# Kernel optimization log

Hardware: AMD Instinct MI355X
Metric: run time of the kernel (lower is better)

Reference implementation:

```python
import jax, jax.numpy as jnp
import numpy as np

B, S, D = 2, 2048, 1024
H, HD = 16, 64


def setup_inputs() -> dict:
    key = jax.random.key(0)
    ks = jax.random.split(key, 10)
    scale = 1.0 / np.sqrt(D)
    inputs_q = jax.random.normal(ks[0], (B, S, D), dtype=jnp.float32)
    inputs_kv = jax.random.normal(ks[1], (B, S, D), dtype=jnp.float32)
    # causal mask, broadcast over batch: True = attend
    mask = jnp.broadcast_to(jnp.tril(jnp.ones((S, S), dtype=bool)), (B, S, S))
    Wq = jax.random.normal(ks[2], (D, H * HD), dtype=jnp.float32) * scale
    bq = jnp.zeros((H * HD,), dtype=jnp.float32)
    Wk = jax.random.normal(ks[3], (D, H * HD), dtype=jnp.float32) * scale
    bk = jnp.zeros((H * HD,), dtype=jnp.float32)
    Wv = jax.random.normal(ks[4], (D, H * HD), dtype=jnp.float32) * scale
    bv = jnp.zeros((H * HD,), dtype=jnp.float32)
    Wo = jax.random.normal(ks[5], (H * HD, D), dtype=jnp.float32) * scale
    bo = jnp.zeros((D,), dtype=jnp.float32)
    return {"inputs_q": inputs_q, "inputs_kv": inputs_kv, "mask": mask,
            "Wq": Wq, "bq": bq, "Wk": Wk, "bk": bk, "Wv": Wv, "bv": bv,
            "Wo": Wo, "bo": bo}


def reference(inputs_q, inputs_kv, mask, Wq, bq, Wk, bk, Wv, bv, Wo, bo):
    b, s_q, _ = inputs_q.shape
    s_k = inputs_kv.shape[1]
    # projections -> [B, S, H, HD]
    q = (inputs_q @ Wq + bq).reshape(b, s_q, H, HD)
    k = (inputs_kv @ Wk + bk).reshape(b, s_k, H, HD)
    v = (inputs_kv @ Wv + bv).reshape(b, s_k, H, HD)
    q = q / jnp.sqrt(jnp.asarray(HD, dtype=q.dtype))
    # scores: [B, H, Sq, Sk]
    attn = jnp.einsum('bqhd,bkhd->bhqk', q, k)
    m = mask[:, None, :, :]  # [B,1,Sq,Sk] broadcast over heads
    attn = jnp.where(m, attn, jnp.asarray(-1e30, dtype=attn.dtype))
    attn = jax.nn.softmax(attn, axis=-1)
    # dropout_rate = 0.0, deterministic -> identity
    out = jnp.einsum('bhqk,bkhd->bqhd', attn, v).reshape(b, s_q, H * HD)
    return out @ Wo + bo
```

## Files before the change

### kernel.cpp

```cpp
#include <hip/hip_runtime.h>

typedef __attribute__((ext_vector_type(4))) float f32x4;
typedef __attribute__((ext_vector_type(8))) short bf16x8;
typedef unsigned short u16;
typedef unsigned int u32;

#define AS1 __attribute__((address_space(1)))
#define AS3 __attribute__((address_space(3)))

#define WAITVM(N) do{ asm volatile("s_waitcnt vmcnt(" #N ")" ::: "memory"); \
                      __builtin_amdgcn_sched_barrier(0); }while(0)
#define RAWBAR    do{ __builtin_amdgcn_s_barrier();                          \
                      __builtin_amdgcn_sched_barrier(0); }while(0)

__device__ __forceinline__ float fast_exp2(float x){
  return __builtin_amdgcn_exp2f(x);
}

__device__ __forceinline__ u16 f2bf(float x){
  u32 u = __float_as_uint(x);
  u += 0x7fffu + ((u >> 16) & 1u);
  return (u16)(u >> 16);
}
__device__ __forceinline__ u16 f2bf_fast(float x){
  return (u16)((__float_as_uint(x) + 0x8000u) >> 16);
}

__global__ __launch_bounds__(256) void prep(const float* __restrict__ W0,
                                            const float* __restrict__ W1,
                                            const float* __restrict__ W2,
                                            const float* __restrict__ W3,
                                            u16* __restrict__ Wt,
                                            const float* __restrict__ inq,
                                            const float* __restrict__ inkv,
                                            u16* __restrict__ Xq,
                                            u16* __restrict__ Xkv)
{
  const int z = blockIdx.z;
  if (z < 4){
    __shared__ float tile[32][33];
    const float* src = z == 0 ? W0 : z == 1 ? W1 : z == 2 ? W2 : W3;
    u16* d = Wt + (size_t)z * 1024 * 1024;
    int tx = threadIdx.x & 31, ty = threadIdx.x >> 5;
    int k0 = blockIdx.x * 32, n0 = blockIdx.y * 32;
    for (int r = 0; r < 4; ++r)
      tile[ty + r * 8][tx] = src[(size_t)(k0 + ty + r * 8) * 1024 + n0 + tx];
    __syncthreads();
    for (int r = 0; r < 4; ++r)
      d[(size_t)(n0 + ty + r * 8) * 1024 + k0 + tx] = f2bf(tile[tx][ty + r * 8]);
  } else {
    const float* src = z == 4 ? inq : inkv;
    u16* dst = z == 4 ? Xq : Xkv;
    int bid = blockIdx.y * 32 + blockIdx.x;
    size_t base4 = ((size_t)bid * 256 + threadIdx.x) * 4;
#pragma unroll
    for (int i = 0; i < 4; ++i){
      float4 v = reinterpret_cast<const float4*>(src)[base4 + i];
      ushort4 o;
      o.x = f2bf(v.x); o.y = f2bf(v.y); o.z = f2bf(v.z); o.w = f2bf(v.w);
      reinterpret_cast<ushort4*>(dst)[base4 + i] = o;
    }
  }
}

__global__ __launch_bounds__(512, 2) void gemm_qkv(const u16* __restrict__ Xq,
                                                   const u16* __restrict__ Xkv,
                                                   const u16* __restrict__ Wt,
                                                   const float* __restrict__ bq,
                                                   const float* __restrict__ bk,
                                                   const float* __restrict__ bv,
                                                   u16* __restrict__ Qb,
                                                   u16* __restrict__ Kb,
                                                   u16* __restrict__ Vt,
                                                   int M, int K)
{
  __shared__ u16 lA[3][256 * 32];
  __shared__ u16 lB[3][256 * 32];
  const int tid = threadIdx.x;
  const int l = tid & 63, w = tid >> 6;
  const int wr = w >> 2, wc = w & 3;
  const int bm0 = blockIdx.x * 256, bn0 = blockIdx.y * 256;
  const int seg = bn0 >> 10;
  const int nloc0 = bn0 & 1023;
  const u16* A = seg ? Xkv : Xq;
  const float* bias = seg == 0 ? bq : seg == 1 ? bk : bv;
  const float scale = seg == 0 ? 0.125f * 1.44269504089f : 1.0f;
  const int lr = l & 15, lg = (l >> 4) * 8;

#define STAGE_G(BI, KK) do{                                                   \
  _Pragma("unroll") for (int c_ = 0; c_ < 2; ++c_){                           \
    int e_ = (c_ * 512 + tid) * 8;                                            \
    int row_ = e_ >> 5, col_ = e_ & 31;                                       \
    __builtin_amdgcn_global_load_lds(                                         \
        (const AS1 u32*)(A + (size_t)(bm0 + row_) * K + (KK) * 32 + col_),    \
        (AS3 u32*)(&lA[BI][e_]), 16, 0, 0);                                   \
    __builtin_amdgcn_global_load_lds(                                         \
        (const AS1 u32*)(Wt + (size_t)(bn0 + row_) * K + (KK) * 32 + col_),   \
        (AS3 u32*)(&lB[BI][e_]), 16, 0, 0);                                   \
  }                                                                           \
}while(0)

  f32x4 acc[8][4];
#pragma unroll
  for (int m = 0; m < 8; ++m)
#pragma unroll
    for (int n = 0; n < 4; ++n) acc[m][n] = (f32x4){0.f, 0.f, 0.f, 0.f};

  STAGE_G(0, 0);
  STAGE_G(1, 1);

#pragma unroll
  for (int k = 0; k < 32; ++k){
    const int cur = k % 3;
    if (k < 30){ STAGE_G((k + 2) % 3, k + 2); WAITVM(8); }
    else if (k == 30){ WAITVM(4); }
    else { WAITVM(0); }
    RAWBAR;

    bf16x8 aF[8], bF[4];
#pragma unroll
    for (int m = 0; m < 8; ++m)
      aF[m] = *reinterpret_cast<const bf16x8*>(&lA[cur][(wr * 128 + m * 16 + lr) * 32 + lg]);
#pragma unroll
    for (int n = 0; n < 4; ++n)
      bF[n] = *reinterpret_cast<const bf16x8*>(&lB[cur][(wc * 64 + n * 16 + lr) * 32 + lg]);
    __builtin_amdgcn_s_setprio(1);
#pragma unroll
    for (int m = 0; m < 8; ++m)
#pragma unroll
      for (int n = 0; n < 4; ++n)
        acc[m][n] = __builtin_amdgcn_mfma_f32_16x16x32_bf16(aF[m], bF[n], acc[m][n], 0, 0, 0);
    __builtin_amdgcn_s_setprio(0);
    RAWBAR;
  }
#undef STAGE_G

  const int r0 = (l >> 4) * 4;
  if (seg < 2){
    u16* C = seg == 0 ? Qb : Kb;
#pragma unroll
    for (int m = 0; m < 8; ++m)
#pragma unroll
      for (int n = 0; n < 4; ++n){
        int col = nloc0 + wc * 64 + n * 16 + lr;
        float bv_ = bias[col];
#pragma unroll
        for (int r = 0; r < 4; ++r){
          int row = bm0 + wr * 128 + m * 16 + r0 + r;
          C[(size_t)row * 1024 + col] = f2bf((acc[m][n][r] + bv_) * scale);
        }
      }
  } else {
#pragma unroll
    for (int m = 0; m < 8; ++m)
#pragma unroll
      for (int n = 0; n < 4; ++n){
        int col = nloc0 + wc * 64 + n * 16 + lr;
        float bv_ = bias[col];
        int h = col >> 6, hdl = col & 63;
#pragma unroll
        for (int r = 0; r < 4; ++r){
          int row = bm0 + wr * 128 + m * 16 + r0 + r;
          int b = row >> 11, kv = row & 2047;
          size_t off = ((size_t)(b * 16 + h)) * 131072 + (size_t)hdl * 2048 + kv;
          Vt[off] = f2bf(acc[m][n][r] + bv_);
        }
      }
  }
}

__global__ __launch_bounds__(256) void gemm_out(const u16* __restrict__ A,
                                                const u16* __restrict__ Bt,
                                                const float* __restrict__ bias,
                                                float* __restrict__ Cf,
                                                int M, int N, int K)
{
  __shared__ u16 lA[3][64 * 32];
  __shared__ u16 lB[3][128 * 32];
  const int tid = threadIdx.x;
  const int l = tid & 63, w = tid >> 6;
  const int wr = w >> 1, wc = w & 1;
  const int bm0 = blockIdx.x * 64, bn0 = blockIdx.y * 128;
  const int lr = l & 15, lg = (l >> 4) * 8;

#define STAGE_O(BI, KK) do{                                                   \
  {                                                                           \
    int e_ = tid * 8;                                                         \
    int row_ = e_ >> 5, col_ = e_ & 31;                                       \
    __builtin_amdgcn_global_load_lds(                                         \
        (const AS1 u32*)(A + (size_t)(bm0 + row_) * K + (KK) * 32 + col_),    \
        (AS3 u32*)(&lA[BI][e_]), 16, 0, 0);                                   \
  }                                                                           \
  _Pragma("unroll") for (int c_ = 0; c_ < 2; ++c_){                           \
    int e_ = (c_ * 256 + tid) * 8;                                            \
    int row_ = e_ >> 5, col_ = e_ & 31;                                       \
    __builtin_amdgcn_global_load_lds(                                         \
        (const AS1 u32*)(Bt + (size_t)(bn0 + row_) * K + (KK) * 32 + col_),   \
        (AS3 u32*)(&lB[BI][e_]), 16, 0, 0);                                   \
  }                                                                           \
}while(0)

  f32x4 acc[2][4];
#pragma unroll
  for (int m = 0; m < 2; ++m)
#pragma unroll
    for (int n = 0; n < 4; ++n) acc[m][n] = (f32x4){0.f, 0.f, 0.f, 0.f};

  STAGE_O(0, 0);
  STAGE_O(1, 1);

#pragma unroll
  for (int k = 0; k < 32; ++k){
    const int cur = k % 3;
    if (k < 30){ STAGE_O((k + 2) % 3, k + 2); WAITVM(6); }
    else if (k == 30){ WAITVM(3); }
    else { WAITVM(0); }
    RAWBAR;

    bf16x8 aF[2], bF[4];
#pragma unroll
    for (int m = 0; m < 2; ++m)
      aF[m] = *reinterpret_cast<const bf16x8*>(&lA[cur][(wr * 32 + m * 16 + lr) * 32 + lg]);
#pragma unroll
    for (int n = 0; n < 4; ++n)
      bF[n] = *reinterpret_cast<const bf16x8*>(&lB[cur][(wc * 64 + n * 16 + lr) * 32 + lg]);
    __builtin_amdgcn_s_setprio(1);
#pragma unroll
    for (int m = 0; m < 2; ++m)
#pragma unroll
      for (int n = 0; n < 4; ++n)
        acc[m][n] = __builtin_amdgcn_mfma_f32_16x16x32_bf16(aF[m], bF[n], acc[m][n], 0, 0, 0);
    __builtin_amdgcn_s_setprio(0);
    RAWBAR;
  }
#undef STAGE_O

  const int r0 = (l >> 4) * 4;
#pragma unroll
  for (int m = 0; m < 2; ++m)
#pragma unroll
    for (int n = 0; n < 4; ++n){
      int col = bn0 + wc * 64 + n * 16 + lr;
      float bv_ = bias[col];
#pragma unroll
      for (int r = 0; r < 4; ++r){
        int row = bm0 + wr * 32 + m * 16 + r0 + r;
        Cf[(size_t)row * N + col] = acc[m][n][r] + bv_;
      }
    }
}

__global__ __launch_bounds__(512, 2) void attn_fwd(const u16* __restrict__ Qb,
                                                   const u16* __restrict__ Kb,
                                                   const u16* __restrict__ Vt,
                                                   u16* __restrict__ AO, int S)
{
  __shared__ u16 lK[2][64 * 64];
  __shared__ u16 lV[2][64 * 64];
  __shared__ u16 lP[8][16 * 72];
  const int tid = threadIdx.x, l = tid & 63, w = tid >> 6;
  const int j = blockIdx.x;
  const int xcd = j & 7;
  const int bh = xcd * 4 + ((j >> 3) & 3);
  const int p = j >> 5;
  const int bb = bh >> 4;
  const size_t baseQK = ((size_t)bb * S) * 1024 + (bh & 15) * 64;
  const u16* gK = Kb + baseQK;
  const u16* gV = Vt + (size_t)bh * 131072;
  const int lr = l & 15, g4 = l >> 4, lg = g4 * 8;

  u16* lPw = (u16*)lP[w];
  bf16x8 ones;
#pragma unroll
  for (int i = 0; i < 8; ++i) ones[i] = (short)0x3F80;

#define STAGE_KV(T, BI) do{                                                   \
  int row_ = tid >> 3, ch_ = tid & 7, sc_ = (ch_ ^ (row_ & 7)) * 8;           \
  __builtin_amdgcn_global_load_lds(                                           \
      (const AS1 u32*)(gK + (size_t)(64 * (T) + row_) * 1024 + sc_),          \
      (AS3 u32*)(&lK[BI][tid * 8]), 16, 0, 0);                                \
  __builtin_amdgcn_global_load_lds(                                           \
      (const AS1 u32*)(gV + (size_t)row_ * 2048 + 64 * (T) + sc_),            \
      (AS3 u32*)(&lV[BI][tid * 8]), 16, 0, 0);                                \
}while(0)

#pragma unroll
  for (int pass = 0; pass < 2; ++pass){
    const int qt = pass ? (15 - p) : p;
    const int ntb = 2 * qt + 2;
    const int q0 = qt * 128 + w * 16;

    bf16x8 qf[2];
#pragma unroll
    for (int kc = 0; kc < 2; ++kc)
      qf[kc] = *reinterpret_cast<const bf16x8*>(
          Qb + baseQK + (size_t)(q0 + lr) * 1024 + kc * 32 + lg);

    f32x4 acc_o[4], acc_l;
    acc_l = (f32x4){0.f, 0.f, 0.f, 0.f};
#pragma unroll
    for (int n = 0; n < 4; ++n) acc_o[n] = (f32x4){0.f, 0.f, 0.f, 0.f};

    int buf = 0;
    STAGE_KV(0, 0);
    for (int t = 0; t < ntb; ++t){
      if (t + 1 < ntb){ STAGE_KV(t + 1, buf ^ 1); WAITVM(2); }
      else            { WAITVM(0); }
      RAWBAR;

      if (64 * t <= q0 + 15){
        const u16* lKb = lK[buf];
        const u16* lVb = lV[buf];
        f32x4 sA[4];
#pragma unroll
        for (int np = 0; np < 4; ++np) sA[np] = (f32x4){0.f, 0.f, 0.f, 0.f};
        __builtin_amdgcn_s_setprio(1);
#pragma unroll
        for (int kc = 0; kc < 2; ++kc)
#pragma unroll
          for (int np = 0; np < 4; ++np){
            int row = np * 16 + lr, ch = kc * 4 + g4;
            bf16x8 kf = *reinterpret_cast<const bf16x8*>(
                reinterpret_cast<const char*>(lKb) + row * 128 + ((ch ^ (row & 7)) << 4));
            sA[np] = __builtin_amdgcn_mfma_f32_16x16x32_bf16(qf[kc], kf, sA[np], 0, 0, 0);
          }
        __builtin_amdgcn_s_setprio(0);

        const bool needmask = (64 * t + 63 > q0);
        if (needmask){
#pragma unroll
          for (int np = 0; np < 4; ++np){
            int kvg = 64 * t + np * 16 + lr;
#pragma unroll
            for (int r = 0; r < 4; ++r){
              int qg = q0 + g4 * 4 + r;
              float e = fast_exp2(sA[np][r]);
              lPw[(g4 * 4 + r) * 72 + np * 16 + lr] = f2bf_fast((kvg <= qg) ? e : 0.f);
            }
          }
        } else {
#pragma unroll
          for (int np = 0; np < 4; ++np)
#pragma unroll
            for (int r = 0; r < 4; ++r)
              lPw[(g4 * 4 + r) * 72 + np * 16 + lr] = f2bf_fast(fast_exp2(sA[np][r]));
        }

        bf16x8 pf[2];
#pragma unroll
        for (int kc = 0; kc < 2; ++kc)
          pf[kc] = *reinterpret_cast<const bf16x8*>(
              reinterpret_cast<const char*>(lPw) + lr * 144 + (kc * 4 + g4) * 16);
        __builtin_amdgcn_s_setprio(1);
#pragma unroll
        for (int kc = 0; kc < 2; ++kc){
          acc_l = __builtin_amdgcn_mfma_f32_16x16x32_bf16(pf[kc], ones, acc_l, 0, 0, 0);
#pragma unroll
          for (int n = 0; n < 4; ++n){
            int row = n * 16 + lr, ch = kc * 4 + g4;
            bf16x8 vf = *reinterpret_cast<const bf16x8*>(
                reinterpret_cast<const char*>(lVb) + row * 128 + ((ch ^ (row & 7)) << 4));
            acc_o[n] = __builtin_amdgcn_mfma_f32_16x16x32_bf16(pf[kc], vf, acc_o[n], 0, 0, 0);
          }
        }
        __builtin_amdgcn_s_setprio(0);
      }
      RAWBAR;
      buf ^= 1;
    }

    float inv[4];
#pragma unroll
    for (int r = 0; r < 4; ++r) inv[r] = 1.0f / acc_l[r];
#pragma unroll
    for (int n = 0; n < 4; ++n)
#pragma unroll
      for (int r = 0; r < 4; ++r){
        int row = q0 + g4 * 4 + r;
        AO[baseQK + (size_t)row * 1024 + n * 16 + lr] = f2bf(acc_o[n][r] * inv[r]);
      }
  }
#undef STAGE_KV
}

extern "C" void kernel_launch(void* const* d_in, const int* in_sizes, int n_in,
                              void* d_out, int out_size, void* d_ws, size_t ws_size,
                              hipStream_t stream)
{
  const float* inq  = (const float*)d_in[0];
  const float* inkv = (const float*)d_in[1];
  const float* Wq = (const float*)d_in[3];
  const float* bq = (const float*)d_in[4];
  const float* Wk = (const float*)d_in[5];
  const float* bk = (const float*)d_in[6];
  const float* Wv = (const float*)d_in[7];
  const float* bv = (const float*)d_in[8];
  const float* Wo = (const float*)d_in[9];
  const float* bo = (const float*)d_in[10];
  float* out = (float*)d_out;

  const int B = 2, S = 2048, D = 1024;
  const int M = B * S;

  char* ws = (char*)d_ws;
  const size_t MB = 1024ull * 1024ull;
  u16* Xq  = (u16*)(ws + 0 * MB);
  u16* Xkv = (u16*)(ws + 8 * MB);
  u16* Wt  = (u16*)(ws + 16 * MB);
  u16* Wot = (u16*)(ws + 22 * MB);
  u16* Qb  = (u16*)(ws + 24 * MB);
  u16* Kb  = (u16*)(ws + 32 * MB);
  u16* Vtg = (u16*)(ws + 40 * MB);
  u16* AOb = (u16*)(ws + 48 * MB);

  prep<<<dim3(32, 32, 6), 256, 0, stream>>>(Wq, Wk, Wv, Wo, Wt, inq, inkv, Xq, Xkv);

  gemm_qkv<<<dim3(M / 256, 3072 / 256), 512, 0, stream>>>(Xq, Xkv, Wt, bq, bk, bv,
                                                          Qb, Kb, Vtg, M, D);

  attn_fwd<<<dim3(256), 512, 0, stream>>>(Qb, Kb, Vtg, AOb, S);

  gemm_out<<<dim3(M / 64, D / 128), 256, 0, stream>>>(AOb, Wot, bo, out, M, D, D);
}
```

Measured before the change: 117.2 us.

## Swizzle LDS tiles in QKV GEMM and split loads across two MFMA halves

The QKV projection GEMM now stores its LDS tiles with an XOR swizzle of the 16-byte chunks within each row, and reads fragments through the matching swizzle, so lanes stop colliding on LDS banks. The K-loop body is split in two halves: the A-tile prefetch is issued before the first half, and the B-tile prefetch is issued between the halves. This spreads global-to-LDS traffic across the MFMA work to overlap it better. In exchange each iteration has an extra barrier and the vmcnt bookkeeping becomes more fragile.

New measurement: 117.0 us. About the same (-0.2%).

```diff
diff --git a/kernel.cpp b/kernel.cpp
--- a/kernel.cpp
+++ b/kernel.cpp
@@ -85,20 +85,31 @@
   const u16* A = seg ? Xkv : Xq;
   const float* bias = seg == 0 ? bq : seg == 1 ? bk : bv;
   const float scale = seg == 0 ? 0.125f * 1.44269504089f : 1.0f;
-  const int lr = l & 15, lg = (l >> 4) * 8;
-
-#define STAGE_G(BI, KK) do{                                                   \
+  const int lr = l & 15, g4 = l >> 4;
+
+#define STAGE_A(BI, KK) do{                                                   \
   _Pragma("unroll") for (int c_ = 0; c_ < 2; ++c_){                           \
-    int e_ = (c_ * 512 + tid) * 8;                                            \
-    int row_ = e_ >> 5, col_ = e_ & 31;                                       \
+    int e_ = c_ * 512 + tid;                                                  \
+    int row_ = e_ >> 2, ch_ = e_ & 3;                                         \
+    int sc_ = (ch_ ^ (row_ & 3)) * 8;                                         \
     __builtin_amdgcn_global_load_lds(                                         \
-        (const AS1 u32*)(A + (size_t)(bm0 + row_) * K + (KK) * 32 + col_),    \
-        (AS3 u32*)(&lA[BI][e_]), 16, 0, 0);                                   \
-    __builtin_amdgcn_global_load_lds(                                         \
-        (const AS1 u32*)(Wt + (size_t)(bn0 + row_) * K + (KK) * 32 + col_),   \
-        (AS3 u32*)(&lB[BI][e_]), 16, 0, 0);                                   \
+        (const AS1 u32*)(A + (size_t)(bm0 + row_) * K + (KK) * 32 + sc_),     \
+        (AS3 u32*)(&lA[BI][e_ * 8]), 16, 0, 0);                               \
   }                                                                           \
 }while(0)
+#define STAGE_B(BI, KK) do{                                                   \
+  _Pragma("unroll") for (int c_ = 0; c_ < 2; ++c_){                           \
+    int e_ = c_ * 512 + tid;                                                  \
+    int row_ = e_ >> 2, ch_ = e_ & 3;                                         \
+    int sc_ = (ch_ ^ (row_ & 3)) * 8;                                         \
+    __builtin_amdgcn_global_load_lds(                                         \
+        (const AS1 u32*)(Wt + (size_t)(bn0 + row_) * K + (KK) * 32 + sc_),    \
+        (AS3 u32*)(&lB[BI][e_ * 8]), 16, 0, 0);                               \
+  }                                                                           \
+}while(0)
+
+#define RD(LDS, ROW) (*reinterpret_cast<const bf16x8*>(                       \
+    reinterpret_cast<const char*>(LDS) + (ROW) * 64 + ((g4 ^ ((ROW) & 3)) << 4)))
 
   f32x4 acc[8][4];
 #pragma unroll
@@ -106,36 +117,52 @@
 #pragma unroll
     for (int n = 0; n < 4; ++n) acc[m][n] = (f32x4){0.f, 0.f, 0.f, 0.f};
 
-  STAGE_G(0, 0);
-  STAGE_G(1, 1);
+  STAGE_A(0, 0); STAGE_B(0, 0);
+  STAGE_A(1, 1); STAGE_B(1, 1);
 
 #pragma unroll
   for (int k = 0; k < 32; ++k){
     const int cur = k % 3;
-    if (k < 30){ STAGE_G((k + 2) % 3, k + 2); WAITVM(8); }
+    if (k < 30){ STAGE_A((k + 2) % 3, k + 2); WAITVM(6); }
     else if (k == 30){ WAITVM(4); }
     else { WAITVM(0); }
     RAWBAR;
 
-    bf16x8 aF[8], bF[4];
-#pragma unroll
-    for (int m = 0; m < 8; ++m)
-      aF[m] = *reinterpret_cast<const bf16x8*>(&lA[cur][(wr * 128 + m * 16 + lr) * 32 + lg]);
+    bf16x8 aLo[4], bF[4];
+#pragma unroll
+    for (int m = 0; m < 4; ++m)
+      aLo[m] = RD(lA[cur], wr * 128 + m * 16 + lr);
 #pragma unroll
     for (int n = 0; n < 4; ++n)
-      bF[n] = *reinterpret_cast<const bf16x8*>(&lB[cur][(wc * 64 + n * 16 + lr) * 32 + lg]);
+      bF[n] = RD(lB[cur], wc * 64 + n * 16 + lr);
     __builtin_amdgcn_s_setprio(1);
 #pragma unroll
-    for (int m = 0; m < 8; ++m)
+    for (int m = 0; m < 4; ++m)
 #pragma unroll
       for (int n = 0; n < 4; ++n)
-        acc[m][n] = __builtin_amdgcn_mfma_f32_16x16x32_bf16(aF[m], bF[n], acc[m][n], 0, 0, 0);
+        acc[m][n] = __builtin_amdgcn_mfma_f32_16x16x32_bf16(aLo[m], bF[n], acc[m][n], 0, 0, 0);
+    __builtin_amdgcn_s_setprio(0);
+    RAWBAR;
+
+    if (k < 30) STAGE_B((k + 2) % 3, k + 2);
+    bf16x8 aHi[4];
+#pragma unroll
+    for (int m = 0; m < 4; ++m)
+      aHi[m] = RD(lA[cur], wr * 128 + (m + 4) * 16 + lr);
+    __builtin_amdgcn_s_setprio(1);
+#pragma unroll
+    for (int m = 0; m < 4; ++m)
+#pragma unroll
+      for (int n = 0; n < 4; ++n)
+        acc[m + 4][n] = __builtin_amdgcn_mfma_f32_16x16x32_bf16(aHi[m], bF[n], acc[m + 4][n], 0, 0, 0);
     __builtin_amdgcn_s_setprio(0);
     RAWBAR;
   }
-#undef STAGE_G
-
-  const int r0 = (l >> 4) * 4;
+#undef STAGE_A
+#undef STAGE_B
+#undef RD
+
+  const int r0 = g4 * 4;
   if (seg < 2){
     u16* C = seg == 0 ? Qb : Kb;
 #pragma unroll
```

## Shrink QKV GEMM tiles to 128x128, add LDS swizzle and XCD-aware block mapping

Applied to the files above, without the earlier changes.

The QKV projection GEMM goes from 256x256 tiles with 512 threads (192 blocks) to 128x128 tiles with 256 threads (768 blocks), so more blocks are available to fill the CUs. Staged LDS data is XOR-swizzled in 16-byte chunks by row to cut bank conflicts on the fragment reads. A 1D grid is remapped so each XCD gets a contiguous set of column tiles, aiming for better L2 reuse of weights. Smaller tiles lower arithmetic intensity and raise global and LDS traffic per flop.

Result: slower. 120.6 us (+2.9%).

```diff
diff --git a/kernel.cpp b/kernel.cpp
--- a/kernel.cpp
+++ b/kernel.cpp
@@ -63,46 +63,54 @@
   }
 }
 
-__global__ __launch_bounds__(512, 2) void gemm_qkv(const u16* __restrict__ Xq,
-                                                   const u16* __restrict__ Xkv,
-                                                   const u16* __restrict__ Wt,
-                                                   const float* __restrict__ bq,
-                                                   const float* __restrict__ bk,
-                                                   const float* __restrict__ bv,
-                                                   u16* __restrict__ Qb,
-                                                   u16* __restrict__ Kb,
-                                                   u16* __restrict__ Vt,
-                                                   int M, int K)
+__global__ __launch_bounds__(256) void gemm_qkv(const u16* __restrict__ Xq,
+                                                const u16* __restrict__ Xkv,
+                                                const u16* __restrict__ Wt,
+                                                const float* __restrict__ bq,
+                                                const float* __restrict__ bk,
+                                                const float* __restrict__ bv,
+                                                u16* __restrict__ Qb,
+                                                u16* __restrict__ Kb,
+                                                u16* __restrict__ Vt,
+                                                int M, int K)
 {
-  __shared__ u16 lA[3][256 * 32];
-  __shared__ u16 lB[3][256 * 32];
+  __shared__ u16 lA[3][128 * 32];
+  __shared__ u16 lB[3][128 * 32];
   const int tid = threadIdx.x;
   const int l = tid & 63, w = tid >> 6;
-  const int wr = w >> 2, wc = w & 3;
-  const int bm0 = blockIdx.x * 256, bn0 = blockIdx.y * 256;
+  const int wr = w >> 1, wc = w & 1;
+  const int j = blockIdx.x;
+  const int xcd = j & 7, idx = j >> 3;
+  const int col_p = xcd * 3 + (idx >> 5);
+  const int row_p = idx & 31;
+  const int bm0 = row_p * 128, bn0 = col_p * 128;
   const int seg = bn0 >> 10;
   const int nloc0 = bn0 & 1023;
   const u16* A = seg ? Xkv : Xq;
   const float* bias = seg == 0 ? bq : seg == 1 ? bk : bv;
   const float scale = seg == 0 ? 0.125f * 1.44269504089f : 1.0f;
-  const int lr = l & 15, lg = (l >> 4) * 8;
+  const int lr = l & 15, g4 = l >> 4;
 
 #define STAGE_G(BI, KK) do{                                                   \
   _Pragma("unroll") for (int c_ = 0; c_ < 2; ++c_){                           \
-    int e_ = (c_ * 512 + tid) * 8;                                            \
-    int row_ = e_ >> 5, col_ = e_ & 31;                                       \
+    int e_ = c_ * 256 + tid;                                                  \
+    int row_ = e_ >> 2, ch_ = e_ & 3;                                         \
+    int sc_ = (ch_ ^ (row_ & 3)) * 8;                                         \
     __builtin_amdgcn_global_load_lds(                                         \
-        (const AS1 u32*)(A + (size_t)(bm0 + row_) * K + (KK) * 32 + col_),    \
-        (AS3 u32*)(&lA[BI][e_]), 16, 0, 0);                                   \
+        (const AS1 u32*)(A + (size_t)(bm0 + row_) * K + (KK) * 32 + sc_),     \
+        (AS3 u32*)(&lA[BI][e_ * 8]), 16, 0, 0);                               \
     __builtin_amdgcn_global_load_lds(                                         \
-        (const AS1 u32*)(Wt + (size_t)(bn0 + row_) * K + (KK) * 32 + col_),   \
-        (AS3 u32*)(&lB[BI][e_]), 16, 0, 0);                                   \
+        (const AS1 u32*)(Wt + (size_t)(bn0 + row_) * K + (KK) * 32 + sc_),    \
+        (AS3 u32*)(&lB[BI][e_ * 8]), 16, 0, 0);                               \
   }                                                                           \
 }while(0)
 
-  f32x4 acc[8][4];
-#pragma unroll
-  for (int m = 0; m < 8; ++m)
+#define RD(LDS, ROW) (*reinterpret_cast<const bf16x8*>(                       \
+    reinterpret_cast<const char*>(LDS) + (ROW) * 64 + ((g4 ^ ((ROW) & 3)) << 4)))
+
+  f32x4 acc[4][4];
+#pragma unroll
+  for (int m = 0; m < 4; ++m)
 #pragma unroll
     for (int n = 0; n < 4; ++n) acc[m][n] = (f32x4){0.f, 0.f, 0.f, 0.f};
 
@@ -117,16 +125,16 @@
     else { WAITVM(0); }
     RAWBAR;
 
-    bf16x8 aF[8], bF[4];
-#pragma unroll
-    for (int m = 0; m < 8; ++m)
-      aF[m] = *reinterpret_cast<const bf16x8*>(&lA[cur][(wr * 128 + m * 16 + lr) * 32 + lg]);
+    bf16x8 aF[4], bF[4];
+#pragma unroll
+    for (int m = 0; m < 4; ++m)
+      aF[m] = RD(lA[cur], wr * 64 + m * 16 + lr);
 #pragma unroll
     for (int n = 0; n < 4; ++n)
-      bF[n] = *reinterpret_cast<const bf16x8*>(&lB[cur][(wc * 64 + n * 16 + lr) * 32 + lg]);
+      bF[n] = RD(lB[cur], wc * 64 + n * 16 + lr);
     __builtin_amdgcn_s_setprio(1);
 #pragma unroll
-    for (int m = 0; m < 8; ++m)
+    for (int m = 0; m < 4; ++m)
 #pragma unroll
       for (int n = 0; n < 4; ++n)
         acc[m][n] = __builtin_amdgcn_mfma_f32_16x16x32_bf16(aF[m], bF[n], acc[m][n], 0, 0, 0);
@@ -134,25 +142,26 @@
     RAWBAR;
   }
 #undef STAGE_G
-
-  const int r0 = (l >> 4) * 4;
+#undef RD
+
+  const int r0 = g4 * 4;
   if (seg < 2){
     u16* C = seg == 0 ? Qb : Kb;
 #pragma unroll
-    for (int m = 0; m < 8; ++m)
+    for (int m = 0; m < 4; ++m)
 #pragma unroll
       for (int n = 0; n < 4; ++n){
         int col = nloc0 + wc * 64 + n * 16 + lr;
         float bv_ = bias[col];
 #pragma unroll
         for (int r = 0; r < 4; ++r){
-          int row = bm0 + wr * 128 + m * 16 + r0 + r;
+          int row = bm0 + wr * 64 + m * 16 + r0 + r;
           C[(size_t)row * 1024 + col] = f2bf((acc[m][n][r] + bv_) * scale);
         }
       }
   } else {
 #pragma unroll
-    for (int m = 0; m < 8; ++m)
+    for (int m = 0; m < 4; ++m)
 #pragma unroll
       for (int n = 0; n < 4; ++n){
         int col = nloc0 + wc * 64 + n * 16 + lr;
@@ -160,7 +169,7 @@
         int h = col >> 6, hdl = col & 63;
 #pragma unroll
         for (int r = 0; r < 4; ++r){
-          int row = bm0 + wr * 128 + m * 16 + r0 + r;
+          int row = bm0 + wr * 64 + m * 16 + r0 + r;
           int b = row >> 11, kv = row & 2047;
           size_t off = ((size_t)(b * 16 + h)) * 131072 + (size_t)hdl * 2048 + kv;
           Vt[off] = f2bf(acc[m][n][r] + bv_);
@@ -415,8 +424,8 @@
 
   prep<<<dim3(32, 32, 6), 256, 0, stream>>>(Wq, Wk, Wv, Wo, Wt, inq, inkv, Xq, Xkv);
 
-  gemm_qkv<<<dim3(M / 256, 3072 / 256), 512, 0, stream>>>(Xq, Xkv, Wt, bq, bk, bv,
-                                                          Qb, Kb, Vtg, M, D);
+  gemm_qkv<<<dim3(768), 256, 0, stream>>>(Xq, Xkv, Wt, bq, bk, bv,
+                                          Qb, Kb, Vtg, M, D);
 
   attn_fwd<<<dim3(256), 512, 0, stream>>>(Qb, Kb, Vtg, AOb, S);
 
```
